# Performance work log

Hardware: AMD Instinct MI355X
Metric: run time of the kernel (lower is better)

Reference implementation:

```python
import jax, jax.numpy as jnp
import numpy as np
import math

B, S, D, H = 2, 2048, 1024, 16
DK = D // H


def setup_inputs() -> dict:
    key = jax.random.key(0)
    ks = jax.random.split(key, 11)
    s = 1.0 / math.sqrt(D)
    return {
        "q": jax.random.normal(ks[0], (B, S, D), jnp.float32),
        "k": jax.random.normal(ks[1], (B, S, D), jnp.float32),
        "v": jax.random.normal(ks[2], (B, S, D), jnp.float32),
        "Wq": jax.random.normal(ks[3], (D, D), jnp.float32) * s,
        "bq": jax.random.normal(ks[4], (D,), jnp.float32) * s,
        "Wk": jax.random.normal(ks[5], (D, D), jnp.float32) * s,
        "bk": jax.random.normal(ks[6], (D,), jnp.float32) * s,
        "Wv": jax.random.normal(ks[7], (D, D), jnp.float32) * s,
        "bv": jax.random.normal(ks[8], (D,), jnp.float32) * s,
        "Wo": jax.random.normal(ks[9], (D, D), jnp.float32) * s,
        "bo": jax.random.normal(ks[10], (D,), jnp.float32) * s,
    }


def reference(q, k, v, Wq, bq, Wk, bk, Wv, bv, Wo, bo):
    bs = q.shape[0]
    # linear projections, split heads: [B, H, S, DK]
    qh = (q @ Wq.T + bq).reshape(bs, -1, H, DK).transpose(0, 2, 1, 3)
    kh = (k @ Wk.T + bk).reshape(bs, -1, H, DK).transpose(0, 2, 1, 3)
    vh = (v @ Wv.T + bv).reshape(bs, -1, H, DK).transpose(0, 2, 1, 3)
    # scaled dot-product attention (dropout in eval mode -> identity)
    scores = jnp.einsum('bhqd,bhkd->bhqk', qh, kh) / math.sqrt(DK)
    attn = jax.nn.softmax(scores, axis=-1)
    out = jnp.einsum('bhqk,bhkd->bhqd', attn, vh)
    concat = out.transpose(0, 2, 1, 3).reshape(bs, -1, D)
    return concat @ Wo.T + bo
```

## Files before the change

kernel.cpp:

```cpp
#include <hip/hip_runtime.h>
#include <stdint.h>

#define DEV __device__ __forceinline__

typedef __bf16 bf16;
typedef __bf16 bf16x8 __attribute__((ext_vector_type(8)));
typedef unsigned short u16x8 __attribute__((ext_vector_type(8)));
typedef unsigned short u16x4 __attribute__((ext_vector_type(4)));
typedef float f32x4 __attribute__((ext_vector_type(4)));
typedef uint32_t u32x4 __attribute__((ext_vector_type(4)));

static constexpr int S = 2048, D = 1024, NH = 16;
static constexpr float QSCALE = 0.125f * 1.44269504088896340736f;
static constexpr float STHR = 4096.0f;

union BU { u16x8 u; bf16x8 v; };
union PU { u32x4 u; bf16x8 v; };

DEV float fexp2(float x) { return __builtin_amdgcn_exp2f(x); }

DEV uint32_t pack2(float a, float b) {
  uint32_t r;
  asm("v_cvt_pk_bf16_f32 %0, %1, %2" : "=v"(r) : "v"(a), "v"(b));
  return r;
}

struct CvtArgs { const float* s[7]; bf16* d[7]; };
__global__ __launch_bounds__(256) void cvt_all(CvtArgs a) {
  int blk = blockIdx.x, seg, rel;
  if (blk < 6144) { seg = blk >> 11; rel = blk & 2047; }
  else { int bb = blk - 6144; seg = 3 + (bb >> 9); rel = bb & 511; }
  int i = rel * 256 + threadIdx.x;
  const float4* p = (const float4*)a.s[seg] + (size_t)i * 2;
  float4 x = p[0], y = p[1];
  u32x4 o;
  o[0] = pack2(x.x, x.y);
  o[1] = pack2(x.z, x.w);
  o[2] = pack2(y.x, y.y);
  o[3] = pack2(y.z, y.w);
  ((u32x4*)a.d[seg])[i] = o;
}

DEV void async_copy16(bf16* lds_dst, const bf16* g_src) {
  __builtin_amdgcn_global_load_lds(
      (const __attribute__((address_space(1))) void*)(g_src),
      (__attribute__((address_space(3))) void*)(lds_dst),
      16, 0, 0);
}

struct GArgs {
  const bf16* A[3]; const bf16* W[3]; const float* bias[3];
  bf16* Cb[3]; float scale[3];
};

__global__ __launch_bounds__(256, 2)
void gemm128(GArgs g) {
  constexpr int N = 1024, K = 1024;
  const int z = blockIdx.z;
  const bf16* A = g.A[z];
  const bf16* Bt = g.W[z];
  const float* bias = g.bias[z];
  const float scale = g.scale[z];

  __shared__ bf16 As[128 * 32];
  __shared__ bf16 Bs[128 * 32];
  const int t = threadIdx.x;
  const int w = t >> 6, l = t & 63;
  const int wr = w >> 1, wc = w & 1;
  const int lr = l & 15, lg = l >> 4;
  const int orig = blockIdx.x + (blockIdx.y << 3);
  const int tl = ((orig & 7) << 5) | (orig >> 3);
  const int m0 = (tl >> 3) * 128, n0 = (tl & 7) * 128;

  f32x4 acc[4][4] = {};

  const int srow = t >> 2, scol = (t & 3) * 8;
  const bf16* Aptr = A + (size_t)(m0 + srow) * K + scol;
  const bf16* Bptr = Bt + (size_t)(n0 + srow) * K + scol;
  bf16* AsDst = &As[w * 512];
  bf16* BsDst = &Bs[w * 512];

  for (int k0 = 0; k0 < K; k0 += 32) {
    async_copy16(AsDst,        Aptr + k0);
    async_copy16(AsDst + 2048, Aptr + (size_t)64 * K + k0);
    async_copy16(BsDst,        Bptr + k0);
    async_copy16(BsDst + 2048, Bptr + (size_t)64 * K + k0);
    __syncthreads();
    bf16x8 af[4], bfr[4];
#pragma unroll
    for (int i = 0; i < 4; i++)
      af[i] = *(const bf16x8*)&As[(wr * 64 + i * 16 + lr) * 32 + lg * 8];
#pragma unroll
    for (int i = 0; i < 4; i++)
      bfr[i] = *(const bf16x8*)&Bs[(wc * 64 + i * 16 + lr) * 32 + lg * 8];
#pragma unroll
    for (int mi = 0; mi < 4; mi++)
#pragma unroll
      for (int ni = 0; ni < 4; ni++)
        acc[mi][ni] = __builtin_amdgcn_mfma_f32_16x16x32_bf16(
            af[mi], bfr[ni], acc[mi][ni], 0, 0, 0);
    __syncthreads();
  }

#pragma unroll
  for (int mi = 0; mi < 4; mi++) {
#pragma unroll
    for (int ni = 0; ni < 4; ni++) {
      int col = n0 + wc * 64 + ni * 16 + lr;
      float bv = bias[col];
#pragma unroll
      for (int r = 0; r < 4; r++) {
        int row = m0 + wr * 64 + mi * 16 + lg * 4 + r;
        uint32_t pk = pack2((acc[mi][ni][r] + bv) * scale, 0.f);
        *(uint16_t*)&g.Cb[z][(size_t)row * N + col] = (uint16_t)pk;
      }
    }
  }
}

__global__ __launch_bounds__(256, 2)
void gemm64out(const bf16* __restrict__ A, const bf16* __restrict__ Bt,
               const float* __restrict__ bias, float* __restrict__ Cf) {
  constexpr int N = 1024, K = 1024;
  __shared__ bf16 As[128 * 32];
  __shared__ bf16 Bs[64 * 32];
  const int t = threadIdx.x;
  const int w = t >> 6, l = t & 63;
  const int lr = l & 15, lg = l >> 4;
  const int orig = blockIdx.x + (blockIdx.y << 4);
  const int tl = ((orig & 7) << 6) | (orig >> 3);
  const int m0 = (tl >> 4) * 128, n0 = (tl & 15) * 64;

  f32x4 acc[2][4] = {};

  const int srow = t >> 2, scol = (t & 3) * 8;
  const bf16* Aptr = A + (size_t)(m0 + srow) * K + scol;
  const bf16* Bptr = Bt + (size_t)(n0 + srow) * K + scol;
  bf16* AsDst = &As[w * 512];
  bf16* BsDst = &Bs[w * 512];

  for (int k0 = 0; k0 < K; k0 += 32) {
    async_copy16(AsDst,        Aptr + k0);
    async_copy16(AsDst + 2048, Aptr + (size_t)64 * K + k0);
    async_copy16(BsDst,        Bptr + k0);
    __syncthreads();
    bf16x8 af[2], bfr[4];
#pragma unroll
    for (int i = 0; i < 2; i++)
      af[i] = *(const bf16x8*)&As[(w * 32 + i * 16 + lr) * 32 + lg * 8];
#pragma unroll
    for (int n = 0; n < 4; n++)
      bfr[n] = *(const bf16x8*)&Bs[(n * 16 + lr) * 32 + lg * 8];
#pragma unroll
    for (int mi = 0; mi < 2; mi++)
#pragma unroll
      for (int ni = 0; ni < 4; ni++)
        acc[mi][ni] = __builtin_amdgcn_mfma_f32_16x16x32_bf16(
            af[mi], bfr[ni], acc[mi][ni], 0, 0, 0);
    __syncthreads();
  }

#pragma unroll
  for (int mi = 0; mi < 2; mi++) {
#pragma unroll
    for (int ni = 0; ni < 4; ni++) {
      int col = n0 + ni * 16 + lr;
      float bv = bias[col];
#pragma unroll
      for (int r = 0; r < 4; r++) {
        int row = m0 + w * 32 + mi * 16 + lg * 4 + r;
        Cf[(size_t)row * N + col] = acc[mi][ni][r] + bv;
      }
    }
  }
}

__global__ __launch_bounds__(512, 4)
void attn_kernel(const bf16* __restrict__ Qp, const bf16* __restrict__ Kp,
                 const bf16* __restrict__ Vp, bf16* __restrict__ Oc) {
  __shared__ uint4 ldsu[2048];
  char* lds = (char*)ldsu;

  const int t = threadIdx.x, w = t >> 6, l = t & 63;
  const int lr = l & 15, lg = l >> 4;
  const int orig = blockIdx.x + (blockIdx.y << 4);
  const int tl = ((orig & 7) << 6) | (orig >> 3);
  const int qblk = tl & 15, bh = tl >> 4;
  const int b = bh >> 4, h = bh & 15;
  const int q0 = qblk * 128;
  const size_t base = (size_t)b * S * D + (size_t)h * 64;
  const size_t TILE = (size_t)64 * D;

  bf16x8 qf[2];
  {
    const bf16* qrow = Qp + base + (size_t)(q0 + w * 16 + lr) * D + lg * 8;
    qf[0] = *(const bf16x8*)(qrow);
    qf[1] = *(const bf16x8*)(qrow + 32);
  }

  f32x4 accO[4] = {};
  float mrun = 4.0f, lsum = 0.f;

  const bf16* kptr;
  {
    int o = t * 16;
    int rho = o >> 7;
    int seg16 = ((o & 127) ^ ((rho & 7) << 4)) >> 4;
    int mm = rho >> 4;
    int srow = ((mm & 1) << 5) | (((rho >> 2) & 3) << 3) | ((mm >> 1) << 2) | (rho & 3);
    kptr = Kp + base + (size_t)srow * D + seg16 * 8;
  }
  bf16* kdst = (bf16*)(lds + w * 1024);

  const int vu = t & 31, vcc = t >> 5;
  const bf16* Vg = Vp + base + (size_t)(2 * vu) * D + vcc * 4;
  int vwa[4];
#pragma unroll
  for (int j = 0; j < 4; j++) {
    int d = vcc * 4 + j;
    vwa[j] = 16384 + ((d * 128 + vu * 4) ^ ((d & 7) << 4));
  }

  const int rswz = (lr & 7) << 4;

  async_copy16(kdst, kptr);
  u16x4 va = *(const u16x4*)(Vg);
  u16x4 vb = *(const u16x4*)(Vg + D);
  __syncthreads();
#pragma unroll
  for (int j = 0; j < 4; j++)
    *(uint32_t*)(lds + vwa[j]) = (uint32_t)va[j] | ((uint32_t)vb[j] << 16);
  va = *(const u16x4*)(Vg + TILE);
  vb = *(const u16x4*)(Vg + TILE + D);
  __syncthreads();

  const bf16* kp1 = kptr + TILE;
  const bf16* vg2 = Vg + 2 * TILE;

#pragma unroll 2
  for (int it = 0; it < 32; ++it) {
    const int cur = (it & 1) * 8192;
    const int nxt = ((it + 1) & 1) * 8192;
    const bool hasN = it < 31, hasN2 = it < 30;

    if (hasN) {
      async_copy16((bf16*)(lds + nxt + w * 1024), kp1);
      kp1 += TILE;
    }
    const bf16* pv = hasN2 ? vg2 : (Vp + base);
    u16x4 ta = *(const u16x4*)(pv);
    u16x4 tb = *(const u16x4*)(pv + D);
    vg2 += TILE;

    f32x4 sc[4] = {};
#pragma unroll
    for (int ks = 0; ks < 2; ks++) {
      BU kf[4];
#pragma unroll
      for (int m = 0; m < 4; m++)
        kf[m].u = *(const u16x8*)(lds + cur +
                   ((((m * 16 + lr) * 128) + ks * 64 + lg * 16) ^ rswz));
      __builtin_amdgcn_s_setprio(1);
#pragma unroll
      for (int m = 0; m < 4; m++)
        sc[m] = __builtin_amdgcn_mfma_f32_16x16x32_bf16(
            kf[m].v, qf[ks], sc[m], 0, 0, 0);
      __builtin_amdgcn_s_setprio(0);
    }

    float s = 0.f;
#pragma unroll
    for (int m = 0; m < 4; m++) {
      sc[m][0] = fexp2(sc[m][0] - mrun);
      sc[m][1] = fexp2(sc[m][1] - mrun);
      sc[m][2] = fexp2(sc[m][2] - mrun);
      sc[m][3] = fexp2(sc[m][3] - mrun);
      s += (sc[m][0] + sc[m][1]) + (sc[m][2] + sc[m][3]);
    }
    if (!__all(s <= STHR)) {
      float pm = sc[0][0];
#pragma unroll
      for (int m = 0; m < 4; m++)
#pragma unroll
        for (int r = 0; r < 4; r++) pm = fmaxf(pm, sc[m][r]);
      pm = fmaxf(pm, __shfl_xor(pm, 16));
      pm = fmaxf(pm, __shfl_xor(pm, 32));
      float mn = fmaxf(mrun + __log2f(pm), mrun);
      float f = fexp2(mrun - mn);
      mrun = mn;
      s *= f;
      lsum *= f;
#pragma unroll
      for (int m = 0; m < 4; m++)
#pragma unroll
        for (int r = 0; r < 4; r++) sc[m][r] *= f;
#pragma unroll
      for (int r = 0; r < 4; r++) {
        float a = __shfl(f, (lg << 4) | (lg * 4 + r));
#pragma unroll
        for (int n = 0; n < 4; n++) accO[n][r] *= a;
      }
    }
    lsum += s;
    uint32_t pk[4][2];
#pragma unroll
    for (int m = 0; m < 4; m++) {
      pk[m][0] = pack2(sc[m][0], sc[m][1]);
      pk[m][1] = pack2(sc[m][2], sc[m][3]);
    }

    if (hasN) {
#pragma unroll
      for (int j = 0; j < 4; j++)
        *(uint32_t*)(lds + vwa[j] + nxt) = (uint32_t)va[j] | ((uint32_t)vb[j] << 16);
    }

#pragma unroll
    for (int ks = 0; ks < 2; ks++) {
      PU pa;
      pa.u[0] = pk[ks][0];
      pa.u[1] = pk[ks][1];
      pa.u[2] = pk[2 + ks][0];
      pa.u[3] = pk[2 + ks][1];
      BU vf[4];
#pragma unroll
      for (int n = 0; n < 4; n++)
        vf[n].u = *(const u16x8*)(lds + 16384 + cur +
                   ((((n * 16 + lr) * 128) + ks * 64 + lg * 16) ^ rswz));
      __builtin_amdgcn_s_setprio(1);
#pragma unroll
      for (int n = 0; n < 4; n++)
        accO[n] = __builtin_amdgcn_mfma_f32_16x16x32_bf16(
            pa.v, vf[n].v, accO[n], 0, 0, 0);
      __builtin_amdgcn_s_setprio(0);
    }

    va = ta; vb = tb;
    __syncthreads();
  }

  lsum += __shfl_xor(lsum, 16);
  lsum += __shfl_xor(lsum, 32);
#pragma unroll
  for (int r = 0; r < 4; r++) {
    float lv = __shfl(lsum, (lg << 4) | (lg * 4 + r));
    float rl = 1.0f / lv;
    int row = q0 + w * 16 + lg * 4 + r;
    bf16* orow = Oc + base + (size_t)row * D;
#pragma unroll
    for (int n = 0; n < 4; n++) {
      uint32_t pkv = pack2(accO[n][r] * rl, 0.f);
      *(uint16_t*)&orow[n * 16 + lr] = (uint16_t)pkv;
    }
  }
}

extern "C" void kernel_launch(void* const* d_in, const int* in_sizes, int n_in,
                              void* d_out, int out_size, void* d_ws, size_t ws_size,
                              hipStream_t stream) {
  const float* q  = (const float*)d_in[0];
  const float* k  = (const float*)d_in[1];
  const float* v  = (const float*)d_in[2];
  const float* Wq = (const float*)d_in[3];
  const float* bq = (const float*)d_in[4];
  const float* Wk = (const float*)d_in[5];
  const float* bk = (const float*)d_in[6];
  const float* Wv = (const float*)d_in[7];
  const float* bv = (const float*)d_in[8];
  const float* Wo = (const float*)d_in[9];
  const float* bo = (const float*)d_in[10];
  float* out = (float*)d_out;

  const int BS = 2 * S;
  const size_t SZ_T = (size_t)BS * D * 2;
  const size_t SZ_W = (size_t)D * D * 2;

  char* ws = (char*)d_ws;
  bf16* qb  = (bf16*)(ws);
  bf16* kb  = (bf16*)(ws + SZ_T);
  bf16* vb  = (bf16*)(ws + 2 * SZ_T);
  bf16* Wqb = (bf16*)(ws + 3 * SZ_T);
  bf16* Wkb = (bf16*)(ws + 3 * SZ_T + SZ_W);
  bf16* Wvb = (bf16*)(ws + 3 * SZ_T + 2 * SZ_W);
  bf16* Wob = (bf16*)(ws + 3 * SZ_T + 3 * SZ_W);
  bf16* Qh  = (bf16*)(ws + 3 * SZ_T + 4 * SZ_W);
  bf16* Kh  = (bf16*)(ws + 4 * SZ_T + 4 * SZ_W);
  bf16* Vh  = (bf16*)(ws + 5 * SZ_T + 4 * SZ_W);
  bf16* Oc  = qb;

  CvtArgs ca;
  ca.s[0] = q;  ca.d[0] = qb;
  ca.s[1] = k;  ca.d[1] = kb;
  ca.s[2] = v;  ca.d[2] = vb;
  ca.s[3] = Wq; ca.d[3] = Wqb;
  ca.s[4] = Wk; ca.d[4] = Wkb;
  ca.s[5] = Wv; ca.d[5] = Wvb;
  ca.s[6] = Wo; ca.d[6] = Wob;
  cvt_all<<<dim3(8192), 256, 0, stream>>>(ca);

  GArgs gp = {};
  gp.A[0] = qb; gp.W[0] = Wqb; gp.bias[0] = bq; gp.Cb[0] = Qh; gp.scale[0] = QSCALE;
  gp.A[1] = kb; gp.W[1] = Wkb; gp.bias[1] = bk; gp.Cb[1] = Kh; gp.scale[1] = 1.0f;
  gp.A[2] = vb; gp.W[2] = Wvb; gp.bias[2] = bv; gp.Cb[2] = Vh; gp.scale[2] = 1.0f;
  gemm128<<<dim3(D / 128, BS / 128, 3), 256, 0, stream>>>(gp);

  attn_kernel<<<dim3(S / 128, 2 * NH), 512, 0, stream>>>(Qh, Kh, Vh, Oc);

  gemm64out<<<dim3(D / 64, BS / 128), 256, 0, stream>>>(Oc, Wob, bo, out);
}
```

Baseline: 214.7 us.

## Double the attention KV tile to 128 keys per iteration

```diff
diff --git a/kernel.cpp b/kernel.cpp
--- a/kernel.cpp
+++ b/kernel.cpp
@@ -6,7 +6,6 @@
 typedef __bf16 bf16;
 typedef __bf16 bf16x8 __attribute__((ext_vector_type(8)));
 typedef unsigned short u16x8 __attribute__((ext_vector_type(8)));
-typedef unsigned short u16x4 __attribute__((ext_vector_type(4)));
 typedef float f32x4 __attribute__((ext_vector_type(4)));
 typedef uint32_t u32x4 __attribute__((ext_vector_type(4)));
 
@@ -24,6 +23,8 @@
   asm("v_cvt_pk_bf16_f32 %0, %1, %2" : "=v"(r) : "v"(a), "v"(b));
   return r;
 }
+DEV float lo_f(uint32_t v) { union { uint32_t u; float f; } c; c.u = v << 16; return c.f; }
+DEV float hi_f(uint32_t v) { union { uint32_t u; float f; } c; c.u = v & 0xffff0000u; return c.f; }
 
 struct CvtArgs { const float* s[7]; bf16* d[7]; };
 __global__ __launch_bounds__(256) void cvt_all(CvtArgs a) {
@@ -178,7 +179,7 @@
 __global__ __launch_bounds__(512, 4)
 void attn_kernel(const bf16* __restrict__ Qp, const bf16* __restrict__ Kp,
                  const bf16* __restrict__ Vp, bf16* __restrict__ Oc) {
-  __shared__ uint4 ldsu[2048];
+  __shared__ uint4 ldsu[4096];
   char* lds = (char*)ldsu;
 
   const int t = threadIdx.x, w = t >> 6, l = t & 63;
@@ -189,7 +190,7 @@
   const int b = bh >> 4, h = bh & 15;
   const int q0 = qblk * 128;
   const size_t base = (size_t)b * S * D + (size_t)h * 64;
-  const size_t TILE = (size_t)64 * D;
+  const size_t TILE = (size_t)128 * D;
 
   bf16x8 qf[2];
   {
@@ -201,88 +202,98 @@
   f32x4 accO[4] = {};
   float mrun = 4.0f, lsum = 0.f;
 
-  const bf16* kptr;
-  {
-    int o = t * 16;
+  const bf16* kptr[2];
+#pragma unroll
+  for (int c = 0; c < 2; c++) {
+    int o = w * 1024 + l * 16;
     int rho = o >> 7;
     int seg16 = ((o & 127) ^ ((rho & 7) << 4)) >> 4;
     int mm = rho >> 4;
     int srow = ((mm & 1) << 5) | (((rho >> 2) & 3) << 3) | ((mm >> 1) << 2) | (rho & 3);
-    kptr = Kp + base + (size_t)srow * D + seg16 * 8;
-  }
-  bf16* kdst = (bf16*)(lds + w * 1024);
-
-  const int vu = t & 31, vcc = t >> 5;
-  const bf16* Vg = Vp + base + (size_t)(2 * vu) * D + vcc * 4;
-  int vwa[4];
-#pragma unroll
-  for (int j = 0; j < 4; j++) {
-    int d = vcc * 4 + j;
-    vwa[j] = 16384 + ((d * 128 + vu * 4) ^ ((d & 7) << 4));
+    kptr[c] = Kp + base + (size_t)(c * 64 + srow) * D + seg16 * 8;
+  }
+
+  const bf16* Vg = Vp + base + (size_t)(2 * l) * D + w * 8;
+  int vwa[8];
+#pragma unroll
+  for (int j = 0; j < 8; j++) {
+    int d = w * 8 + j;
+    vwa[j] = 32768 + ((d * 256 + l * 4) ^ ((d & 7) << 4));
   }
 
   const int rswz = (lr & 7) << 4;
 
-  async_copy16(kdst, kptr);
-  u16x4 va = *(const u16x4*)(Vg);
-  u16x4 vb = *(const u16x4*)(Vg + D);
+  async_copy16((bf16*)(lds + w * 1024),        kptr[0]);
+  async_copy16((bf16*)(lds + 8192 + w * 1024), kptr[1]);
+  u16x8 va = *(const u16x8*)(Vg);
+  u16x8 vb = *(const u16x8*)(Vg + D);
   __syncthreads();
 #pragma unroll
-  for (int j = 0; j < 4; j++)
+  for (int j = 0; j < 8; j++)
     *(uint32_t*)(lds + vwa[j]) = (uint32_t)va[j] | ((uint32_t)vb[j] << 16);
-  va = *(const u16x4*)(Vg + TILE);
-  vb = *(const u16x4*)(Vg + TILE + D);
+  va = *(const u16x8*)(Vg + TILE);
+  vb = *(const u16x8*)(Vg + TILE + D);
   __syncthreads();
 
-  const bf16* kp1 = kptr + TILE;
+  const bf16* kp0 = kptr[0] + TILE;
+  const bf16* kp1 = kptr[1] + TILE;
   const bf16* vg2 = Vg + 2 * TILE;
 
-#pragma unroll 2
-  for (int it = 0; it < 32; ++it) {
-    const int cur = (it & 1) * 8192;
-    const int nxt = ((it + 1) & 1) * 8192;
-    const bool hasN = it < 31, hasN2 = it < 30;
+  for (int it = 0; it < 16; ++it) {
+    const int cur = (it & 1) * 16384;
+    const int nxt = ((it + 1) & 1) * 16384;
+    const bool hasN = it < 15, hasN2 = it < 14;
 
     if (hasN) {
-      async_copy16((bf16*)(lds + nxt + w * 1024), kp1);
-      kp1 += TILE;
+      async_copy16((bf16*)(lds + nxt + w * 1024),        kp0);
+      async_copy16((bf16*)(lds + nxt + 8192 + w * 1024), kp1);
+      kp0 += TILE; kp1 += TILE;
     }
     const bf16* pv = hasN2 ? vg2 : (Vp + base);
-    u16x4 ta = *(const u16x4*)(pv);
-    u16x4 tb = *(const u16x4*)(pv + D);
+    u16x8 ta = *(const u16x8*)(pv);
+    u16x8 tb = *(const u16x8*)(pv + D);
     vg2 += TILE;
 
-    f32x4 sc[4] = {};
-#pragma unroll
-    for (int ks = 0; ks < 2; ks++) {
-      BU kf[4];
-#pragma unroll
-      for (int m = 0; m < 4; m++)
-        kf[m].u = *(const u16x8*)(lds + cur +
-                   ((((m * 16 + lr) * 128) + ks * 64 + lg * 16) ^ rswz));
-      __builtin_amdgcn_s_setprio(1);
-#pragma unroll
-      for (int m = 0; m < 4; m++)
-        sc[m] = __builtin_amdgcn_mfma_f32_16x16x32_bf16(
-            kf[m].v, qf[ks], sc[m], 0, 0, 0);
-      __builtin_amdgcn_s_setprio(0);
-    }
-
     float s = 0.f;
-#pragma unroll
-    for (int m = 0; m < 4; m++) {
-      sc[m][0] = fexp2(sc[m][0] - mrun);
-      sc[m][1] = fexp2(sc[m][1] - mrun);
-      sc[m][2] = fexp2(sc[m][2] - mrun);
-      sc[m][3] = fexp2(sc[m][3] - mrun);
-      s += (sc[m][0] + sc[m][1]) + (sc[m][2] + sc[m][3]);
-    }
+    uint32_t pk[8][2];
+#pragma unroll
+    for (int hh = 0; hh < 2; hh++) {
+      f32x4 sc[4] = {};
+#pragma unroll
+      for (int ks = 0; ks < 2; ks++) {
+        BU kf[4];
+#pragma unroll
+        for (int m = 0; m < 4; m++)
+          kf[m].u = *(const u16x8*)(lds + cur + hh * 8192 +
+                     ((((m * 16 + lr) * 128) + ks * 64 + lg * 16) ^ rswz));
+        __builtin_amdgcn_s_setprio(1);
+#pragma unroll
+        for (int m = 0; m < 4; m++)
+          sc[m] = __builtin_amdgcn_mfma_f32_16x16x32_bf16(
+              kf[m].v, qf[ks], sc[m], 0, 0, 0);
+        __builtin_amdgcn_s_setprio(0);
+      }
+#pragma unroll
+      for (int m = 0; m < 4; m++) {
+        float p0 = fexp2(sc[m][0] - mrun);
+        float p1 = fexp2(sc[m][1] - mrun);
+        float p2 = fexp2(sc[m][2] - mrun);
+        float p3 = fexp2(sc[m][3] - mrun);
+        s += (p0 + p1) + (p2 + p3);
+        pk[hh * 4 + m][0] = pack2(p0, p1);
+        pk[hh * 4 + m][1] = pack2(p2, p3);
+      }
+    }
+
     if (!__all(s <= STHR)) {
-      float pm = sc[0][0];
-#pragma unroll
-      for (int m = 0; m < 4; m++)
-#pragma unroll
-        for (int r = 0; r < 4; r++) pm = fmaxf(pm, sc[m][r]);
+      float pm = 0.f;
+#pragma unroll
+      for (int m = 0; m < 8; m++)
+#pragma unroll
+        for (int d2 = 0; d2 < 2; d2++) {
+          pm = fmaxf(pm, lo_f(pk[m][d2]));
+          pm = fmaxf(pm, hi_f(pk[m][d2]));
+        }
       pm = fmaxf(pm, __shfl_xor(pm, 16));
       pm = fmaxf(pm, __shfl_xor(pm, 32));
       float mn = fmaxf(mrun + __log2f(pm), mrun);
@@ -291,9 +302,10 @@
       s *= f;
       lsum *= f;
 #pragma unroll
-      for (int m = 0; m < 4; m++)
-#pragma unroll
-        for (int r = 0; r < 4; r++) sc[m][r] *= f;
+      for (int m = 0; m < 8; m++)
+#pragma unroll
+        for (int d2 = 0; d2 < 2; d2++)
+          pk[m][d2] = pack2(lo_f(pk[m][d2]) * f, hi_f(pk[m][d2]) * f);
 #pragma unroll
       for (int r = 0; r < 4; r++) {
         float a = __shfl(f, (lg << 4) | (lg * 4 + r));
@@ -302,38 +314,34 @@
       }
     }
     lsum += s;
-    uint32_t pk[4][2];
-#pragma unroll
-    for (int m = 0; m < 4; m++) {
-      pk[m][0] = pack2(sc[m][0], sc[m][1]);
-      pk[m][1] = pack2(sc[m][2], sc[m][3]);
-    }
 
     if (hasN) {
 #pragma unroll
-      for (int j = 0; j < 4; j++)
+      for (int j = 0; j < 8; j++)
         *(uint32_t*)(lds + vwa[j] + nxt) = (uint32_t)va[j] | ((uint32_t)vb[j] << 16);
     }
 
 #pragma unroll
-    for (int ks = 0; ks < 2; ks++) {
-      PU pa;
-      pa.u[0] = pk[ks][0];
-      pa.u[1] = pk[ks][1];
-      pa.u[2] = pk[2 + ks][0];
-      pa.u[3] = pk[2 + ks][1];
-      BU vf[4];
-#pragma unroll
-      for (int n = 0; n < 4; n++)
-        vf[n].u = *(const u16x8*)(lds + 16384 + cur +
-                   ((((n * 16 + lr) * 128) + ks * 64 + lg * 16) ^ rswz));
-      __builtin_amdgcn_s_setprio(1);
-#pragma unroll
-      for (int n = 0; n < 4; n++)
-        accO[n] = __builtin_amdgcn_mfma_f32_16x16x32_bf16(
-            pa.v, vf[n].v, accO[n], 0, 0, 0);
-      __builtin_amdgcn_s_setprio(0);
-    }
+    for (int hh = 0; hh < 2; hh++)
+#pragma unroll
+      for (int ks = 0; ks < 2; ks++) {
+        PU pa;
+        pa.u[0] = pk[hh * 4 + ks][0];
+        pa.u[1] = pk[hh * 4 + ks][1];
+        pa.u[2] = pk[hh * 4 + 2 + ks][0];
+        pa.u[3] = pk[hh * 4 + 2 + ks][1];
+        BU vf[4];
+#pragma unroll
+        for (int n = 0; n < 4; n++)
+          vf[n].u = *(const u16x8*)(lds + 32768 + cur +
+                     ((((n * 16 + lr) * 256) + hh * 128 + ks * 64 + lg * 16) ^ rswz));
+        __builtin_amdgcn_s_setprio(1);
+#pragma unroll
+        for (int n = 0; n < 4; n++)
+          accO[n] = __builtin_amdgcn_mfma_f32_16x16x32_bf16(
+              pa.v, vf[n].v, accO[n], 0, 0, 0);
+        __builtin_amdgcn_s_setprio(0);
+      }
 
     va = ta; vb = tb;
     __syncthreads();
```

Measured after the change: 216.6 us. Within noise of the previous version (+0.9%).
